# Performance work log

Hardware: AMD Instinct MI355X
Metric: run time of the kernel (lower is better)

The kernel has to match this reference:

```python
import jax, jax.numpy as jnp
import numpy as np

M = 16
C = 7 * M          # 112, stage-8 channels
CLS = 20
TOPK = 3
NQ = 20000         # current-frame active sites at stage 8
NS = 8192          # support-frame active sites at stage 8
SCALE = 128.0      # voxel coordinate range at this depth


def setup_inputs() -> dict:
    key = jax.random.key(0)
    ks = jax.random.split(key, 9)
    coords_q = jax.random.uniform(ks[0], (NQ, 3), jnp.float32) * SCALE
    coords_s = jax.random.uniform(ks[1], (NS, 3), jnp.float32) * SCALE
    x7 = jax.random.normal(ks[2], (NQ, C), jnp.float32)
    feat_s7 = jax.random.normal(ks[3], (NS, C), jnp.float32)
    feat_s = jax.random.normal(ks[4], (NS, C), jnp.float32)
    w_attn = jax.random.normal(ks[5], (C,), jnp.float32) * 0.1
    W1 = jax.random.normal(ks[6], (2 * C, C), jnp.float32) * (1.0 / np.sqrt(2 * C))
    gamma = jnp.ones((C,), jnp.float32)
    beta = jnp.zeros((C,), jnp.float32)
    W2 = jax.random.normal(ks[7], (C, C), jnp.float32) * (1.0 / np.sqrt(C))
    W_cls = jax.random.normal(ks[8], (C, CLS), jnp.float32) * (1.0 / np.sqrt(C))
    b_cls = jnp.zeros((CLS,), jnp.float32)
    return dict(coords_q=coords_q, coords_s=coords_s, x7=x7, feat_s7=feat_s7,
                feat_s=feat_s, w_attn=w_attn, W1=W1, gamma=gamma, beta=beta,
                W2=W2, W_cls=W_cls, b_cls=b_cls)


def reference(coords_q, coords_s, x7, feat_s7, feat_s, w_attn, W1, gamma, beta, W2, W_cls, b_cls):
    # GlobalMeanAttentionPooling: attention-weighted mean over support sites -> global vector [C]
    a = jax.nn.softmax(feat_s7 @ w_attn)          # [NS]
    g = a @ feat_s7                                # [C]
    # GlobalMaskLayer: channel-wise sigmoid gating of current-frame features
    feat_q = x7 * jax.nn.sigmoid(g)                # [NQ, C]
    # DistMatchLayer_v4: top-3 nearest support voxels per query, softmax(-d2) weighting
    q2 = jnp.sum(coords_q * coords_q, -1, keepdims=True)   # [NQ, 1]
    s2 = jnp.sum(coords_s * coords_s, -1)                  # [NS]
    d2 = q2 + s2[None, :] - 2.0 * (coords_q @ coords_s.T)  # [NQ, NS]
    negd, idx = jax.lax.top_k(-d2, TOPK)                   # [NQ, K]
    w = jax.nn.softmax(negd, axis=-1)                      # [NQ, K]
    matched = jnp.einsum('nk,nkc->nc', w, feat_s[idx])     # [NQ, C]
    # tune_sub: 1x1 subconv (14m->7m) -> BN(eval affine) + ReLU -> 1x1 subconv (7m->7m)
    h = jnp.concatenate([feat_q, matched], -1) @ W1        # [NQ, C]
    h = jax.nn.relu(h * gamma + beta) @ W2                 # [NQ, C]
    # final classifier linear
    return h @ W_cls + b_cls                               # [NQ, CLS]
```

## Files before the change

### kernel.cpp

```cpp
#include <hip/hip_runtime.h>

#define NQv 20000
#define NSv 8192
#define Cv  112
#define CLSv 20
#define INFF 3.4e38f
#define JINF 0x7fffffff

#define GC 16
#define NCELL 4096
#define CELLH 8.0f
#define INVH 0.125f

#define POOLB 32
#define PT 1024
#define PNW (POOLB * PT / 64)

#define MQ 32
#define MB (NQv / MQ)
#define MT 512
#define WS_START 3616
#define WS_PTS4  5668
#define WS_W1TH  38440
#define WS_W1TL  50984
#define WS_W2TH  63528
#define WS_W2TL  70696
#define WS_WCT   77864

typedef __attribute__((ext_vector_type(8))) short bf16x8;
typedef __attribute__((ext_vector_type(4))) float f32x4;
typedef unsigned short us;
typedef unsigned long long u64;

__device__ __forceinline__ float bf2f(us u) {
    union { unsigned int i; float f; } v; v.i = ((unsigned int)u) << 16; return v.f;
}
__device__ __forceinline__ us f2bf(float f) {
    union { float f; unsigned int i; } v; v.f = f;
    unsigned int r = v.i + 0x7fffu + ((v.i >> 16) & 1u);
    return (us)(r >> 16);
}
__device__ __forceinline__ void split(float v, us& h, us& l) {
    h = f2bf(v); l = f2bf(v - bf2f(h));
}

__device__ __forceinline__ u64 mkkey(float e, int j) {
    union { float f; unsigned int i; } v; v.f = e;
    unsigned int ue = v.i ^ ((unsigned int)((int)v.i >> 31) | 0x80000000u);
    return ((u64)ue << 32) | (unsigned int)j;
}
__device__ __forceinline__ float keyval(u64 k) {
    unsigned int ue = (unsigned int)(k >> 32);
    unsigned int u = ue ^ ((unsigned int)((int)(~ue) >> 31) | 0x80000000u);
    union { unsigned int i; float f; } v; v.i = u; return v.f;
}
__device__ __forceinline__ u64 umin64(u64 a, u64 b) { return a < b ? a : b; }
__device__ __forceinline__ u64 umax64(u64 a, u64 b) { return a > b ? a : b; }

__global__ __launch_bounds__(PT) void k_prep(const float* __restrict__ cs,
                                             const float* __restrict__ fs7,
                                             const float* __restrict__ wat,
                                             const float* __restrict__ W1,
                                             const float* __restrict__ W2,
                                             const float* __restrict__ Wc,
                                             float* __restrict__ ws) {
    int b = blockIdx.x, tid = threadIdx.x;

    if (b == POOLB + 1) {
        us* w1h = (us*)(ws + WS_W1TH);
        us* w1l = (us*)(ws + WS_W1TL);
        for (int idx = tid; idx < Cv * 224; idx += PT) {
            int c = idx / 224, k = idx - c * 224;
            us h, l; split(W1[k * Cv + c], h, l);
            w1h[c * 224 + k] = h; w1l[c * 224 + k] = l;
        }
        return;
    }
    if (b == POOLB + 2) {
        us* w2h = (us*)(ws + WS_W2TH);
        us* w2l = (us*)(ws + WS_W2TL);
        for (int idx = tid; idx < Cv * 128; idx += PT) {
            int c = idx >> 7, k = idx & 127;
            float v = (k < Cv) ? W2[k * Cv + c] : 0.f;
            us h, l; split(v, h, l);
            w2h[c * 128 + k] = h; w2l[c * 128 + k] = l;
        }
        float* wct = ws + WS_WCT;
        for (int idx = tid; idx < CLSv * Cv; idx += PT) {
            int cls = idx / Cv, k = idx - cls * Cv;
            wct[cls * Cv + k] = Wc[k * CLSv + cls];
        }
        return;
    }
    if (b == POOLB) {
        __shared__ int cnt[NCELL];
        __shared__ int wsum[PT / 64];
        us* startg = (us*)(ws + WS_START);
        float4* pts4 = (float4*)(ws + WS_PTS4);
        int lane = tid & 63, wv = tid >> 6;
        for (int i = tid; i < NCELL; i += PT) cnt[i] = 0;
        __syncthreads();
        float xx[8], yy[8], zz[8]; int cid[8]; int pp[8];
        #pragma unroll
        for (int k = 0; k < NSv / PT; ++k) {
            int p = k * PT + tid;
            pp[k] = p;
            xx[k] = cs[3 * p]; yy[k] = cs[3 * p + 1]; zz[k] = cs[3 * p + 2];
            int cx = (int)(xx[k] * INVH), cy = (int)(yy[k] * INVH), cz = (int)(zz[k] * INVH);
            cx = cx > 15 ? 15 : cx; cy = cy > 15 ? 15 : cy; cz = cz > 15 ? 15 : cz;
            cid[k] = (cz * GC + cy) * GC + cx;
            atomicAdd(&cnt[cid[k]], 1);
        }
        __syncthreads();
        int base = tid * 4;
        int c0 = cnt[base], c1 = cnt[base + 1], c2 = cnt[base + 2], c3 = cnt[base + 3];
        int local = c0 + c1 + c2 + c3;
        int inc = local;
        #pragma unroll
        for (int off = 1; off < 64; off <<= 1) {
            int v = __shfl_up(inc, off, 64);
            if (lane >= off) inc += v;
        }
        if (lane == 63) wsum[wv] = inc;
        __syncthreads();
        if (tid < PT / 64) {
            int v = wsum[tid];
            #pragma unroll
            for (int off = 1; off < 16; off <<= 1) {
                int o = __shfl_up(v, off, 64);
                if (tid >= off) v += o;
            }
            wsum[tid] = v;
        }
        __syncthreads();
        int wbase = (wv == 0) ? 0 : wsum[wv - 1];
        int run = wbase + inc - local;
        startg[base] = (us)run;     cnt[base] = run;     run += c0;
        startg[base + 1] = (us)run; cnt[base + 1] = run; run += c1;
        startg[base + 2] = (us)run; cnt[base + 2] = run; run += c2;
        startg[base + 3] = (us)run; cnt[base + 3] = run;
        if (tid == 0) startg[NCELL] = (us)NSv;
        __syncthreads();
        #pragma unroll
        for (int k = 0; k < NSv / PT; ++k) {
            int slot = atomicAdd(&cnt[cid[k]], 1);
            pts4[slot] = make_float4(-2.f * xx[k], -2.f * yy[k], -2.f * zz[k], (float)pp[k]);
        }
        return;
    }

    __shared__ float red[PT / 64][Cv + 1];
    int gtid = b * PT + tid;
    int wid = gtid >> 6, lw = tid >> 6, lane = gtid & 63, l2 = lane * 2;
    float2 wa = make_float2(0.f, 0.f);
    if (lane < 56) wa = *(const float2*)(wat + l2);
    float gx = 0.f, gy = 0.f, z = 0.f;
    for (int g = 0; g < 2; ++g) {
        float2 f[8]; float part[8];
        #pragma unroll
        for (int u = 0; u < 8; ++u) {
            int i = wid + (g * 8 + u) * PNW;
            f[u] = (lane < 56) ? *(const float2*)(fs7 + i * Cv + l2) : make_float2(0.f, 0.f);
            part[u] = f[u].x * wa.x + f[u].y * wa.y;
        }
        #pragma unroll
        for (int off = 32; off; off >>= 1)
            #pragma unroll
            for (int u = 0; u < 8; ++u) part[u] += __shfl_xor(part[u], off, 64);
        #pragma unroll
        for (int u = 0; u < 8; ++u) {
            float p = __expf(part[u]);
            gx = fmaf(p, f[u].x, gx); gy = fmaf(p, f[u].y, gy); z += p;
        }
    }
    if (lane < 56) { red[lw][l2] = gx; red[lw][l2 + 1] = gy; }
    if (lane == 0) red[lw][Cv] = z;
    __syncthreads();
    if (tid < Cv + 1) {
        float s = 0.f;
        #pragma unroll
        for (int i = 0; i < PT / 64; ++i) s += red[i][tid];
        ws[tid * POOLB + b] = s;
    }
}

__device__ __forceinline__ void ins_pt(float4 P, float qx, float qy, float qz,
                                       float& E0, float& E1, float& E2,
                                       int& J0, int& J1, int& J2) {
    float x = -0.5f * P.x, y = -0.5f * P.y, z = -0.5f * P.z;
    float s2 = fmaf(x, x, fmaf(y, y, z * z));
    float e = fmaf(qx, P.x, fmaf(qy, P.y, fmaf(qz, P.z, s2)));
    int j = (int)P.w;
    bool lt2 = (e < E2) || (e == E2 && j < J2);
    if (lt2) {
        bool lt1 = (e < E1) || (e == E1 && j < J1);
        bool lt0 = (e < E0) || (e == E0 && j < J0);
        E2 = lt1 ? E1 : e;              J2 = lt1 ? J1 : j;
        E1 = lt0 ? E0 : (lt1 ? e : E1); J1 = lt0 ? J0 : (lt1 ? j : J1);
        if (lt0) { E0 = e; J0 = j; }
    }
}

__device__ __forceinline__ void scan_run(const float4* __restrict__ pts4,
                                         int a, int b, float qx, float qy, float qz,
                                         float& E0, float& E1, float& E2,
                                         int& J0, int& J1, int& J2) {
    int k = a;
    for (; k + 2 <= b; k += 2) {
        float4 P0 = pts4[k];
        float4 P1 = pts4[k + 1];
        ins_pt(P0, qx, qy, qz, E0, E1, E2, J0, J1, J2);
        ins_pt(P1, qx, qy, qz, E0, E1, E2, J0, J1, J2);
    }
    if (k < b) {
        float4 P0 = pts4[k];
        ins_pt(P0, qx, qy, qz, E0, E1, E2, J0, J1, J2);
    }
}

__global__ __launch_bounds__(MT, 6) void k_fused(
        const float* __restrict__ cq,
        const float* __restrict__ x7, const float* __restrict__ fs,
        const float* __restrict__ gma, const float* __restrict__ bta,
        const float* __restrict__ bc, const float* __restrict__ ws,
        float* __restrict__ out) {
    __shared__ __align__(16) us vb[2 * MQ * 232];
    __shared__ __align__(16) us hbh[MQ * 136];
    __shared__ __align__(16) us hbl[MQ * 136];
    __shared__ float gate[Cv];

    us* vbh = vb;
    us* vbl = vb + MQ * 232;
    float* h2f = (float*)vb;

    const us* __restrict__ startg = (const us*)(ws + WS_START);
    const float4* __restrict__ pts4 = (const float4*)(ws + WS_PTS4);

    int tid = threadIdx.x;
    int q0 = blockIdx.x * MQ;
    int sub = tid & 15;
    int qq  = tid >> 4;
    int q   = q0 + qq;

    float4 px[4];
    if (sub < 7) {
        const float4* xr = (const float4*)(x7 + q * Cv + sub * 16);
        px[0] = xr[0]; px[1] = xr[1]; px[2] = xr[2]; px[3] = xr[3];
    }

    if (tid < Cv) {
        float st = 0.f, zt = 0.f;
        const float* pr = ws + tid * POOLB;
        const float* zr = ws + Cv * POOLB;
        #pragma unroll
        for (int b = 0; b < POOLB; ++b) { st += pr[b]; zt += zr[b]; }
        gate[tid] = 1.0f / (1.0f + __expf(-(st / zt)));
    }
    {
        int zq = tid >> 4, kk = Cv + (tid & 15);
        hbh[zq * 136 + kk] = 0; hbl[zq * 136 + kk] = 0;
    }
    __syncthreads();

    u64 K0 = ~0ull, K1 = ~0ull, K2 = ~0ull;
    {
        float qx = cq[3 * q], qy = cq[3 * q + 1], qz = cq[3 * q + 2];
        float q2 = fmaf(qx, qx, fmaf(qy, qy, qz * qz));
        int cx = (int)(qx * INVH), cy = (int)(qy * INVH), cz = (int)(qz * INVH);
        cx = cx > 15 ? 15 : cx; cy = cy > 15 ? 15 : cy; cz = cz > 15 ? 15 : cz;
        float E0 = INFF, E1 = INFF, E2 = INFF;
        int   J0 = JINF, J1 = JINF, J2 = JINF;

        #pragma unroll
        for (int c = sub; c < 27; c += 16) {
            int dz = c / 9 - 1, dy = (c / 3) % 3 - 1, dx = c % 3 - 1;
            int xc = cx + dx, yc = cy + dy, zc = cz + dz;
            if ((unsigned)xc < 16u && (unsigned)yc < 16u && (unsigned)zc < 16u) {
                int ccell = (zc * GC + yc) * GC + xc;
                scan_run(pts4, startg[ccell], startg[ccell + 1], qx, qy, qz,
                         E0, E1, E2, J0, J1, J2);
            }
        }

        bool done = false;
        for (int s = 2; ; ++s) {
            if (!done) {
                K0 = mkkey(E0, J0); K1 = mkkey(E1, J1); K2 = mkkey(E2, J2);
                #pragma unroll
                for (int off = 1; off < 16; off <<= 1) {
                    u64 b0 = __shfl_xor(K0, off, 64);
                    u64 b1 = __shfl_xor(K1, off, 64);
                    u64 b2 = __shfl_xor(K2, off, 64);
                    u64 xx = umax64(K0, b0), yy = umin64(K1, b1);
                    u64 zz = umax64(K1, b1), uu = umin64(K2, b2);
                    K0 = umin64(K0, b0);
                    u64 n1 = umin64(xx, yy);
                    K2 = umin64(umin64(umax64(xx, yy), zz), uu);
                    K1 = n1;
                }
            }
            if (s > 15) break;
            if (!done) {
                int r = s - 1;
                int xl = cx - r > 0 ? cx - r : 0, xh = cx + r < 15 ? cx + r : 15;
                int yl = cy - r > 0 ? cy - r : 0, yh = cy + r < 15 ? cy + r : 15;
                int zl = cz - r > 0 ? cz - r : 0, zh = cz + r < 15 ? cz + r : 15;
                float fx = INFF, fy = INFF, fz = INFF;
                if (xl > 0)  fx = qx - xl * CELLH;
                if (xh < 15) fx = fminf(fx, (xh + 1) * CELLH - qx);
                if (yl > 0)  fy = qy - yl * CELLH;
                if (yh < 15) fy = fminf(fy, (yh + 1) * CELLH - qy);
                if (zl > 0)  fz = qz - zl * CELLH;
                if (zh < 15) fz = fminf(fz, (zh + 1) * CELLH - qz);
                float dmin = fminf(fx, fminf(fy, fz));
                float t2 = keyval(K2);
                if (dmin * dmin > t2 + q2 + 0.5f) {
                    done = true;
                } else if (s == 2) {
                    for (int idx = sub; idx < 125; idx += 16) {
                        int dz = idx / 25 - 2;
                        int rem = idx - (dz + 2) * 25;
                        int dy = rem / 5 - 2;
                        int dx = rem - (dy + 2) * 5 - 2;
                        int ax = dx < 0 ? -dx : dx, ay = dy < 0 ? -dy : dy, az = dz < 0 ? -dz : dz;
                        if (ax != 2 && ay != 2 && az != 2) continue;
                        int xc = cx + dx, yc = cy + dy, zc = cz + dz;
                        if ((unsigned)xc > 15u || (unsigned)yc > 15u || (unsigned)zc > 15u) continue;
                        int ccell = (zc * GC + yc) * GC + xc;
                        scan_run(pts4, startg[ccell], startg[ccell + 1], qx, qy, qz,
                                 E0, E1, E2, J0, J1, J2);
                    }
                } else {
                    int side = 2 * s + 1, s2n = side * side, tot = s2n * side;
                    for (int idx = sub; idx < tot; idx += 16) {
                        int dz = idx / s2n - s;
                        int rem = idx - (dz + s) * s2n;
                        int dy = rem / side - s;
                        int dx = rem - (dy + s) * side - s;
                        int ax = dx < 0 ? -dx : dx, ay = dy < 0 ? -dy : dy, az = dz < 0 ? -dz : dz;
                        if (ax != s && ay != s && az != s) continue;
                        int xc = cx + dx, yc = cy + dy, zc = cz + dz;
                        if ((unsigned)xc > 15u || (unsigned)yc > 15u || (unsigned)zc > 15u) continue;
                        int ccell = (zc * GC + yc) * GC + xc;
                        scan_run(pts4, startg[ccell], startg[ccell + 1], qx, qy, qz,
                                 E0, E1, E2, J0, J1, J2);
                    }
                }
            }
            if (__all(done)) break;
        }
    }

    {
        unsigned int A0 = (unsigned int)K0;
        unsigned int A1 = (unsigned int)K1;
        unsigned int A2 = (unsigned int)K2;
        if (A0 >= NSv) A0 = 0;
        if (A1 >= NSv) A1 = 0;
        if (A2 >= NSv) A2 = 0;
        if (sub < 7) {
            int k0 = sub * 16;
            const float4* g4 = (const float4*)(gate + k0);
            float vals[16];
            #pragma unroll
            for (int i = 0; i < 4; ++i) {
                float4 v = px[i], g = g4[i];
                vals[i * 4]     = v.x * g.x;
                vals[i * 4 + 1] = v.y * g.y;
                vals[i * 4 + 2] = v.z * g.z;
                vals[i * 4 + 3] = v.w * g.w;
            }
            #pragma unroll
            for (int i = 0; i < 16; ++i) {
                us h, l; split(vals[i], h, l);
                vbh[qq * 232 + k0 + i] = h;
                vbl[qq * 232 + k0 + i] = l;
            }
        } else if (sub < 14) {
            float e0 = keyval(K0), e1 = keyval(K1), e2 = keyval(K2);
            float w1v = __expf(e0 - e1);
            float w2v = __expf(e0 - e2);
            float iw  = 1.0f / (1.0f + w1v + w2v);
            float w0 = iw, w1 = w1v * iw, w2 = w2v * iw;
            int kk = (sub - 7) * 16;
            const float4* r0 = (const float4*)(fs + A0 * Cv + kk);
            const float4* r1 = (const float4*)(fs + A1 * Cv + kk);
            const float4* r2 = (const float4*)(fs + A2 * Cv + kk);
            float vals[16];
            #pragma unroll
            for (int i = 0; i < 4; ++i) {
                float4 a = r0[i], b = r1[i], c = r2[i];
                vals[i * 4]     = w0 * a.x + w1 * b.x + w2 * c.x;
                vals[i * 4 + 1] = w0 * a.y + w1 * b.y + w2 * c.y;
                vals[i * 4 + 2] = w0 * a.z + w1 * b.z + w2 * c.z;
                vals[i * 4 + 3] = w0 * a.w + w1 * b.w + w2 * c.w;
            }
            int k0 = Cv + kk;
            #pragma unroll
            for (int i = 0; i < 16; ++i) {
                us h, l; split(vals[i], h, l);
                vbh[qq * 232 + k0 + i] = h;
                vbl[qq * 232 + k0 + i] = l;
            }
        }
    }
    __syncthreads();

    int w = tid >> 6, lane = tid & 63, quad = lane >> 4, l16 = lane & 15;
    int cc = (w < 7 ? w : 0) * 16 + l16;

    if (w < 7) {
        f32x4 acc0 = {0.f, 0.f, 0.f, 0.f};
        f32x4 acc1 = {0.f, 0.f, 0.f, 0.f};
        const us* w1h = (const us*)(ws + WS_W1TH) + cc * 224;
        const us* w1l = (const us*)(ws + WS_W1TL) + cc * 224;
        #pragma unroll
        for (int ks = 0; ks < 7; ++ks) {
            int ko = ks * 32 + quad * 8;
            bf16x8 bh  = *(const bf16x8*)(w1h + ko);
            bf16x8 bl  = *(const bf16x8*)(w1l + ko);
            bf16x8 a0h = *(const bf16x8*)(vbh + l16 * 232 + ko);
            bf16x8 a0l = *(const bf16x8*)(vbl + l16 * 232 + ko);
            bf16x8 a1h = *(const bf16x8*)(vbh + (l16 + 16) * 232 + ko);
            bf16x8 a1l = *(const bf16x8*)(vbl + (l16 + 16) * 232 + ko);
            acc0 = __builtin_amdgcn_mfma_f32_16x16x32_bf16(a0h, bh, acc0, 0, 0, 0);
            acc0 = __builtin_amdgcn_mfma_f32_16x16x32_bf16(a0l, bh, acc0, 0, 0, 0);
            acc0 = __builtin_amdgcn_mfma_f32_16x16x32_bf16(a0h, bl, acc0, 0, 0, 0);
            acc1 = __builtin_amdgcn_mfma_f32_16x16x32_bf16(a1h, bh, acc1, 0, 0, 0);
            acc1 = __builtin_amdgcn_mfma_f32_16x16x32_bf16(a1l, bh, acc1, 0, 0, 0);
            acc1 = __builtin_amdgcn_mfma_f32_16x16x32_bf16(a1h, bl, acc1, 0, 0, 0);
        }
        float g = gma[cc], bb = bta[cc];
        #pragma unroll
        for (int r = 0; r < 4; ++r) {
            int dq = quad * 4 + r;
            float h = fmaf(acc0[r], g, bb); h = h > 0.f ? h : 0.f;
            us hh, ll; split(h, hh, ll);
            hbh[dq * 136 + cc] = hh; hbl[dq * 136 + cc] = ll;
            float h2 = fmaf(acc1[r], g, bb); h2 = h2 > 0.f ? h2 : 0.f;
            split(h2, hh, ll);
            hbh[(dq + 16) * 136 + cc] = hh; hbl[(dq + 16) * 136 + cc] = ll;
        }
    }
    __syncthreads();

    if (w < 7) {
        f32x4 acc0 = {0.f, 0.f, 0.f, 0.f};
        f32x4 acc1 = {0.f, 0.f, 0.f, 0.f};
        const us* w2h = (const us*)(ws + WS_W2TH) + cc * 128;
        const us* w2l = (const us*)(ws + WS_W2TL) + cc * 128;
        #pragma unroll
        for (int ks = 0; ks < 4; ++ks) {
            int ko = ks * 32 + quad * 8;
            bf16x8 bh  = *(const bf16x8*)(w2h + ko);
            bf16x8 bl  = *(const bf16x8*)(w2l + ko);
            bf16x8 a0h = *(const bf16x8*)(hbh + l16 * 136 + ko);
            bf16x8 a0l = *(const bf16x8*)(hbl + l16 * 136 + ko);
            bf16x8 a1h = *(const bf16x8*)(hbh + (l16 + 16) * 136 + ko);
            bf16x8 a1l = *(const bf16x8*)(hbl + (l16 + 16) * 136 + ko);
            acc0 = __builtin_amdgcn_mfma_f32_16x16x32_bf16(a0h, bh, acc0, 0, 0, 0);
            acc0 = __builtin_amdgcn_mfma_f32_16x16x32_bf16(a0l, bh, acc0, 0, 0, 0);
            acc0 = __builtin_amdgcn_mfma_f32_16x16x32_bf16(a0h, bl, acc0, 0, 0, 0);
            acc1 = __builtin_amdgcn_mfma_f32_16x16x32_bf16(a1h, bh, acc1, 0, 0, 0);
            acc1 = __builtin_amdgcn_mfma_f32_16x16x32_bf16(a1l, bh, acc1, 0, 0, 0);
            acc1 = __builtin_amdgcn_mfma_f32_16x16x32_bf16(a1h, bl, acc1, 0, 0, 0);
        }
        #pragma unroll
        for (int r = 0; r < 4; ++r) {
            int dq = quad * 4 + r;
            h2f[dq * 116 + cc] = acc0[r];
            h2f[(dq + 16) * 116 + cc] = acc1[r];
        }
    }
    __syncthreads();

    for (int it = tid; it < MQ * CLSv; it += MT) {
        int cls = it % CLSv, oq = it / CLSv;
        const float4* wr = (const float4*)(ws + WS_WCT + cls * Cv);
        const float4* hr = (const float4*)(h2f + oq * 116);
        float a = bc[cls];
        #pragma unroll 7
        for (int i = 0; i < 28; ++i) {
            float4 h = hr[i], v = wr[i];
            a = fmaf(h.x, v.x, fmaf(h.y, v.y, fmaf(h.z, v.z, fmaf(h.w, v.w, a))));
        }
        out[(q0 + oq) * CLSv + cls] = a;
    }
}

extern "C" void kernel_launch(void* const* d_in, const int* in_sizes, int n_in,
                              void* d_out, int out_size, void* d_ws, size_t ws_size,
                              hipStream_t stream) {
    const float* cq  = (const float*)d_in[0];
    const float* cs  = (const float*)d_in[1];
    const float* x7  = (const float*)d_in[2];
    const float* fs7 = (const float*)d_in[3];
    const float* fs  = (const float*)d_in[4];
    const float* wat = (const float*)d_in[5];
    const float* W1  = (const float*)d_in[6];
    const float* gma = (const float*)d_in[7];
    const float* bta = (const float*)d_in[8];
    const float* W2  = (const float*)d_in[9];
    const float* Wc  = (const float*)d_in[10];
    const float* bc  = (const float*)d_in[11];
    float* ws  = (float*)d_ws;
    float* out = (float*)d_out;

    k_prep<<<POOLB + 3, PT, 0, stream>>>(cs, fs7, wat, W1, W2, Wc, ws);
    k_fused<<<MB, MT, 0, stream>>>(cq, x7, fs, gma, bta, bc, ws, out);
}
```

Measured before the change: 142.0 us.

## Double block threads to 32 lanes per query and split MFMA tiles across 14 waves

Raises the block size from 512 to 1024 threads, so each query gets 32 cooperating lanes instead of 16. Each lane scans at most one of the 27 neighbour cells, the shell loops stride by 32, and the top-3 shuffle reduction widens to 32 lanes. Feature staging now moves 8 channels per lane instead of 16. The two MLP GEMMs are spread over 14 waves that each own one 16-row M tile, instead of 7 waves handling both tiles. This adds parallelism to the latency-bound neighbour search, at the cost of a wider reduction, more idle lanes in sparse shells, and tighter per-thread register limits under the new launch bounds.

```diff
diff --git a/kernel.cpp b/kernel.cpp
--- a/kernel.cpp
+++ b/kernel.cpp
@@ -18,7 +18,7 @@
 
 #define MQ 32
 #define MB (NQv / MQ)
-#define MT 512
+#define MT 1024
 #define WS_START 3616
 #define WS_PTS4  5668
 #define WS_W1TH  38440
@@ -218,7 +218,7 @@
     }
 }
 
-__global__ __launch_bounds__(MT, 6) void k_fused(
+__global__ __launch_bounds__(MT, 8) void k_fused(
         const float* __restrict__ cq,
         const float* __restrict__ x7, const float* __restrict__ fs,
         const float* __restrict__ gma, const float* __restrict__ bta,
@@ -238,14 +238,14 @@
 
     int tid = threadIdx.x;
     int q0 = blockIdx.x * MQ;
-    int sub = tid & 15;
-    int qq  = tid >> 4;
+    int sub = tid & 31;
+    int qq  = tid >> 5;
     int q   = q0 + qq;
 
-    float4 px[4];
-    if (sub < 7) {
-        const float4* xr = (const float4*)(x7 + q * Cv + sub * 16);
-        px[0] = xr[0]; px[1] = xr[1]; px[2] = xr[2]; px[3] = xr[3];
+    float4 px[2];
+    if (sub < 14) {
+        const float4* xr = (const float4*)(x7 + q * Cv + sub * 8);
+        px[0] = xr[0]; px[1] = xr[1];
     }
 
     if (tid < Cv) {
@@ -256,7 +256,7 @@
         for (int b = 0; b < POOLB; ++b) { st += pr[b]; zt += zr[b]; }
         gate[tid] = 1.0f / (1.0f + __expf(-(st / zt)));
     }
-    {
+    if (tid < MQ * 16) {
         int zq = tid >> 4, kk = Cv + (tid & 15);
         hbh[zq * 136 + kk] = 0; hbl[zq * 136 + kk] = 0;
     }
@@ -271,9 +271,8 @@
         float E0 = INFF, E1 = INFF, E2 = INFF;
         int   J0 = JINF, J1 = JINF, J2 = JINF;
 
-        #pragma unroll
-        for (int c = sub; c < 27; c += 16) {
-            int dz = c / 9 - 1, dy = (c / 3) % 3 - 1, dx = c % 3 - 1;
+        if (sub < 27) {
+            int dz = sub / 9 - 1, dy = (sub / 3) % 3 - 1, dx = sub % 3 - 1;
             int xc = cx + dx, yc = cy + dy, zc = cz + dz;
             if ((unsigned)xc < 16u && (unsigned)yc < 16u && (unsigned)zc < 16u) {
                 int ccell = (zc * GC + yc) * GC + xc;
@@ -287,7 +286,7 @@
             if (!done) {
                 K0 = mkkey(E0, J0); K1 = mkkey(E1, J1); K2 = mkkey(E2, J2);
                 #pragma unroll
-                for (int off = 1; off < 16; off <<= 1) {
+                for (int off = 1; off < 32; off <<= 1) {
                     u64 b0 = __shfl_xor(K0, off, 64);
                     u64 b1 = __shfl_xor(K1, off, 64);
                     u64 b2 = __shfl_xor(K2, off, 64);
@@ -317,7 +316,7 @@
                 if (dmin * dmin > t2 + q2 + 0.5f) {
                     done = true;
                 } else if (s == 2) {
-                    for (int idx = sub; idx < 125; idx += 16) {
+                    for (int idx = sub; idx < 125; idx += 32) {
                         int dz = idx / 25 - 2;
                         int rem = idx - (dz + 2) * 25;
                         int dy = rem / 5 - 2;
@@ -332,7 +331,7 @@
                     }
                 } else {
                     int side = 2 * s + 1, s2n = side * side, tot = s2n * side;
-                    for (int idx = sub; idx < tot; idx += 16) {
+                    for (int idx = sub; idx < tot; idx += 32) {
                         int dz = idx / s2n - s;
                         int rem = idx - (dz + s) * s2n;
                         int dy = rem / side - s;
@@ -358,12 +357,12 @@
         if (A0 >= NSv) A0 = 0;
         if (A1 >= NSv) A1 = 0;
         if (A2 >= NSv) A2 = 0;
-        if (sub < 7) {
-            int k0 = sub * 16;
+        if (sub < 14) {
+            int k0 = sub * 8;
             const float4* g4 = (const float4*)(gate + k0);
-            float vals[16];
-            #pragma unroll
-            for (int i = 0; i < 4; ++i) {
+            float vals[8];
+            #pragma unroll
+            for (int i = 0; i < 2; ++i) {
                 float4 v = px[i], g = g4[i];
                 vals[i * 4]     = v.x * g.x;
                 vals[i * 4 + 1] = v.y * g.y;
@@ -371,24 +370,24 @@
                 vals[i * 4 + 3] = v.w * g.w;
             }
             #pragma unroll
-            for (int i = 0; i < 16; ++i) {
+            for (int i = 0; i < 8; ++i) {
                 us h, l; split(vals[i], h, l);
                 vbh[qq * 232 + k0 + i] = h;
                 vbl[qq * 232 + k0 + i] = l;
             }
-        } else if (sub < 14) {
+        } else if (sub < 28) {
             float e0 = keyval(K0), e1 = keyval(K1), e2 = keyval(K2);
             float w1v = __expf(e0 - e1);
             float w2v = __expf(e0 - e2);
             float iw  = 1.0f / (1.0f + w1v + w2v);
             float w0 = iw, w1 = w1v * iw, w2 = w2v * iw;
-            int kk = (sub - 7) * 16;
+            int kk = (sub - 14) * 8;
             const float4* r0 = (const float4*)(fs + A0 * Cv + kk);
             const float4* r1 = (const float4*)(fs + A1 * Cv + kk);
             const float4* r2 = (const float4*)(fs + A2 * Cv + kk);
-            float vals[16];
-            #pragma unroll
-            for (int i = 0; i < 4; ++i) {
+            float vals[8];
+            #pragma unroll
+            for (int i = 0; i < 2; ++i) {
                 float4 a = r0[i], b = r1[i], c = r2[i];
                 vals[i * 4]     = w0 * a.x + w1 * b.x + w2 * c.x;
                 vals[i * 4 + 1] = w0 * a.y + w1 * b.y + w2 * c.y;
@@ -397,7 +396,7 @@
             }
             int k0 = Cv + kk;
             #pragma unroll
-            for (int i = 0; i < 16; ++i) {
+            for (int i = 0; i < 8; ++i) {
                 us h, l; split(vals[i], h, l);
                 vbh[qq * 232 + k0 + i] = h;
                 vbl[qq * 232 + k0 + i] = l;
@@ -407,69 +406,55 @@
     __syncthreads();
 
     int w = tid >> 6, lane = tid & 63, quad = lane >> 4, l16 = lane & 15;
-    int cc = (w < 7 ? w : 0) * 16 + l16;
-
-    if (w < 7) {
-        f32x4 acc0 = {0.f, 0.f, 0.f, 0.f};
-        f32x4 acc1 = {0.f, 0.f, 0.f, 0.f};
+    int ct = (w < 14) ? (w >> 1) : 0;
+    int mt = (w & 1) * 16;
+    int cc = ct * 16 + l16;
+
+    if (w < 14) {
+        f32x4 acc = {0.f, 0.f, 0.f, 0.f};
         const us* w1h = (const us*)(ws + WS_W1TH) + cc * 224;
         const us* w1l = (const us*)(ws + WS_W1TL) + cc * 224;
         #pragma unroll
         for (int ks = 0; ks < 7; ++ks) {
             int ko = ks * 32 + quad * 8;
-            bf16x8 bh  = *(const bf16x8*)(w1h + ko);
-            bf16x8 bl  = *(const bf16x8*)(w1l + ko);
-            bf16x8 a0h = *(const bf16x8*)(vbh + l16 * 232 + ko);
-            bf16x8 a0l = *(const bf16x8*)(vbl + l16 * 232 + ko);
-            bf16x8 a1h = *(const bf16x8*)(vbh + (l16 + 16) * 232 + ko);
-            bf16x8 a1l = *(const bf16x8*)(vbl + (l16 + 16) * 232 + ko);
-            acc0 = __builtin_amdgcn_mfma_f32_16x16x32_bf16(a0h, bh, acc0, 0, 0, 0);
-            acc0 = __builtin_amdgcn_mfma_f32_16x16x32_bf16(a0l, bh, acc0, 0, 0, 0);
-            acc0 = __builtin_amdgcn_mfma_f32_16x16x32_bf16(a0h, bl, acc0, 0, 0, 0);
-            acc1 = __builtin_amdgcn_mfma_f32_16x16x32_bf16(a1h, bh, acc1, 0, 0, 0);
-            acc1 = __builtin_amdgcn_mfma_f32_16x16x32_bf16(a1l, bh, acc1, 0, 0, 0);
-            acc1 = __builtin_amdgcn_mfma_f32_16x16x32_bf16(a1h, bl, acc1, 0, 0, 0);
+            bf16x8 bh = *(const bf16x8*)(w1h + ko);
+            bf16x8 bl = *(const bf16x8*)(w1l + ko);
+            bf16x8 ah = *(const bf16x8*)(vbh + (mt + l16) * 232 + ko);
+            bf16x8 al = *(const bf16x8*)(vbl + (mt + l16) * 232 + ko);
+            acc = __builtin_amdgcn_mfma_f32_16x16x32_bf16(ah, bh, acc, 0, 0, 0);
+            acc = __builtin_amdgcn_mfma_f32_16x16x32_bf16(al, bh, acc, 0, 0, 0);
+            acc = __builtin_amdgcn_mfma_f32_16x16x32_bf16(ah, bl, acc, 0, 0, 0);
         }
         float g = gma[cc], bb = bta[cc];
         #pragma unroll
         for (int r = 0; r < 4; ++r) {
-            int dq = quad * 4 + r;
-            float h = fmaf(acc0[r], g, bb); h = h > 0.f ? h : 0.f;
+            int dq = mt + quad * 4 + r;
+            float h = fmaf(acc[r], g, bb); h = h > 0.f ? h : 0.f;
             us hh, ll; split(h, hh, ll);
             hbh[dq * 136 + cc] = hh; hbl[dq * 136 + cc] = ll;
-            float h2 = fmaf(acc1[r], g, bb); h2 = h2 > 0.f ? h2 : 0.f;
-            split(h2, hh, ll);
-            hbh[(dq + 16) * 136 + cc] = hh; hbl[(dq + 16) * 136 + cc] = ll;
         }
     }
     __syncthreads();
 
-    if (w < 7) {
-        f32x4 acc0 = {0.f, 0.f, 0.f, 0.f};
-        f32x4 acc1 = {0.f, 0.f, 0.f, 0.f};
+    if (w < 14) {
+        f32x4 acc = {0.f, 0.f, 0.f, 0.f};
         const us* w2h = (const us*)(ws + WS_W2TH) + cc * 128;
         const us* w2l = (const us*)(ws + WS_W2TL) + cc * 128;
         #pragma unroll
         for (int ks = 0; ks < 4; ++ks) {
             int ko = ks * 32 + quad * 8;
-            bf16x8 bh  = *(const bf16x8*)(w2h + ko);
-            bf16x8 bl  = *(const bf16x8*)(w2l + ko);
-            bf16x8 a0h = *(const bf16x8*)(hbh + l16 * 136 + ko);
-            bf16x8 a0l = *(const bf16x8*)(hbl + l16 * 136 + ko);
-            bf16x8 a1h = *(const bf16x8*)(hbh + (l16 + 16) * 136 + ko);
-            bf16x8 a1l = *(const bf16x8*)(hbl + (l16 + 16) * 136 + ko);
-            acc0 = __builtin_amdgcn_mfma_f32_16x16x32_bf16(a0h, bh, acc0, 0, 0, 0);
-            acc0 = __builtin_amdgcn_mfma_f32_16x16x32_bf16(a0l, bh, acc0, 0, 0, 0);
-            acc0 = __builtin_amdgcn_mfma_f32_16x16x32_bf16(a0h, bl, acc0, 0, 0, 0);
-            acc1 = __builtin_amdgcn_mfma_f32_16x16x32_bf16(a1h, bh, acc1, 0, 0, 0);
-            acc1 = __builtin_amdgcn_mfma_f32_16x16x32_bf16(a1l, bh, acc1, 0, 0, 0);
-            acc1 = __builtin_amdgcn_mfma_f32_16x16x32_bf16(a1h, bl, acc1, 0, 0, 0);
+            bf16x8 bh = *(const bf16x8*)(w2h + ko);
+            bf16x8 bl = *(const bf16x8*)(w2l + ko);
+            bf16x8 ah = *(const bf16x8*)(hbh + (mt + l16) * 136 + ko);
+            bf16x8 al = *(const bf16x8*)(hbl + (mt + l16) * 136 + ko);
+            acc = __builtin_amdgcn_mfma_f32_16x16x32_bf16(ah, bh, acc, 0, 0, 0);
+            acc = __builtin_amdgcn_mfma_f32_16x16x32_bf16(al, bh, acc, 0, 0, 0);
+            acc = __builtin_amdgcn_mfma_f32_16x16x32_bf16(ah, bl, acc, 0, 0, 0);
         }
         #pragma unroll
         for (int r = 0; r < 4; ++r) {
-            int dq = quad * 4 + r;
-            h2f[dq * 116 + cc] = acc0[r];
-            h2f[(dq + 16) * 116 + cc] = acc1[r];
+            int dq = mt + quad * 4 + r;
+            h2f[dq * 116 + cc] = acc[r];
         }
     }
     __syncthreads();
```

Result: slower. 156.0 us (+9.8%).
